# Kernel optimization log

Hardware: AMD Instinct MI355X
Metric: run time of the kernel (lower is better)

Reference implementation:

```python
import jax, jax.numpy as jnp
import numpy as np

B, N, D_IN, D_OUT = 2, 2048, 2048, 2048
H, G = 16, 4            # num_heads, n_kv_groups
HD = D_OUT // H         # head_dim = 128
REP = H // G            # query heads per kv head = 4


def setup_inputs() -> dict:
    key = jax.random.key(0)
    ks = jax.random.split(key, 6)
    s = lambda fan_in: 1.0 / np.sqrt(fan_in)
    return {
        "x": jax.random.normal(ks[0], (B, N, D_IN), jnp.float32),
        "Wq": jax.random.normal(ks[1], (D_IN, D_OUT), jnp.float32) * s(D_IN),
        "Wk": jax.random.normal(ks[2], (D_IN, G * HD), jnp.float32) * s(D_IN),
        "Wv": jax.random.normal(ks[3], (D_IN, G * HD), jnp.float32) * s(D_IN),
        "Wo": jax.random.normal(ks[4], (D_OUT, D_OUT), jnp.float32) * s(D_OUT),
        "bo": jnp.zeros((D_OUT,), jnp.float32),
    }


def reference(x, Wq, Wk, Wv, Wo, bo):
    b, n, _ = x.shape
    # projections
    q = (x @ Wq).reshape(b, n, G, REP, HD)   # query heads grouped: h = g*REP + r
    k = (x @ Wk).reshape(b, n, G, HD)
    v = (x @ Wv).reshape(b, n, G, HD)
    # grouped attention scores; KV broadcast over REP instead of repeat_kv
    scores = jnp.einsum('bqgrd,bkgd->bgrqk', q, k)  # [b,G,REP,N,N]
    causal = jnp.tril(jnp.ones((n, n), bool))       # allowed positions
    scores = jnp.where(causal, scores, -jnp.inf)
    w = jax.nn.softmax(scores / np.float32(np.sqrt(HD)), axis=-1)
    ctx = jnp.einsum('bgrqk,bkgd->bqgrd', w, v).reshape(b, n, D_OUT)
    return ctx @ Wo + bo
```

## Files before the change

kernel.cpp:

```cpp
#include <hip/hip_runtime.h>
#include <stdint.h>

typedef __attribute__((ext_vector_type(8))) __bf16 bf16x8;
typedef __attribute__((ext_vector_type(4))) float f32x4;
typedef __attribute__((ext_vector_type(4))) short short4v;

static constexpr int SEQ  = 2048;
static constexpr int DQKV = 3072;
static constexpr int HD   = 128;

__device__ __forceinline__ short f2bf(float f) {
  unsigned u = __builtin_bit_cast(unsigned, f);
  u += 0x7fffu + ((u >> 16) & 1u);
  return (short)(u >> 16);
}

__device__ __forceinline__ unsigned pack2(float a, float b) {
  return (unsigned)(unsigned short)f2bf(a) | ((unsigned)(unsigned short)f2bf(b) << 16);
}

__device__ __forceinline__ void gl_lds16(const void* g, void* l) {
  __builtin_amdgcn_global_load_lds(
      (const __attribute__((address_space(1))) void*)g,
      (__attribute__((address_space(3))) void*)l, 16, 0, 0);
}

__global__ __launch_bounds__(256)
void prep_kernel(const float* __restrict__ x, const float* __restrict__ Wq,
                 const float* __restrict__ Wk, const float* __restrict__ Wv,
                 const float* __restrict__ Wo,
                 short* __restrict__ xb, short* __restrict__ WqkvT,
                 short* __restrict__ WoT) {
  int blk = blockIdx.x, tid = threadIdx.x;
  if (blk < 8192) {
    int i = blk * 256 + tid;
    float4 v = reinterpret_cast<const float4*>(x)[i];
    short4v o;
    o[0] = f2bf(v.x); o[1] = f2bf(v.y); o[2] = f2bf(v.z); o[3] = f2bf(v.w);
    *reinterpret_cast<short4v*>(xb + (size_t)i * 4) = o;
    return;
  }
  blk -= 8192;
  __shared__ float tile[32][33];
  const float* in; short* out; int C, bx, by;
  if (blk < 4096)      { in = Wq; out = WqkvT;                     C = 2048; bx = blk & 63; by = blk >> 6; }
  else if (blk < 5120) { int t = blk - 4096; in = Wk; out = WqkvT + (size_t)2048 * 2048; C = 512; bx = t & 15; by = t >> 4; }
  else if (blk < 6144) { int t = blk - 5120; in = Wv; out = WqkvT + (size_t)2560 * 2048; C = 512; bx = t & 15; by = t >> 4; }
  else                 { int t = blk - 6144; in = Wo; out = WoT;   C = 2048; bx = t & 63; by = t >> 6; }
  const int R = 2048;
  int c0 = bx * 32, r0 = by * 32, tx = tid & 31, ty = tid >> 5;
  for (int i = 0; i < 4; i++)
    tile[ty + i * 8][tx] = in[(size_t)(r0 + ty + i * 8) * C + c0 + tx];
  __syncthreads();
  for (int i = 0; i < 4; i++)
    out[(size_t)(c0 + ty + i * 8) * R + r0 + tx] = f2bf(tile[tx][ty + i * 8]);
}

__global__ __launch_bounds__(256) void transpose_v_kernel(const short* __restrict__ qkv,
                                                          short* __restrict__ vT) {
  __shared__ short tile[32][33];
  int n0 = blockIdx.x * 32, c0 = blockIdx.y * 32, b = blockIdx.z;
  int tx = threadIdx.x & 31, ty = threadIdx.x >> 5;
  for (int i = 0; i < 4; i++)
    tile[ty + i * 8][tx] = qkv[(size_t)(b * SEQ + n0 + ty + i * 8) * DQKV + 2560 + c0 + tx];
  __syncthreads();
  for (int i = 0; i < 4; i++)
    vT[(size_t)(b * 512 + c0 + ty + i * 8) * SEQ + n0 + tx] = tile[tx][ty + i * 8];
}

template <int F32OUT>
__global__ __launch_bounds__(256)
void gemm_bt_kernel(const short* __restrict__ A, const short* __restrict__ BT,
                    void* __restrict__ Cout, const float* __restrict__ bias,
                    int M, int N, int K, int qcols, float qscale) {
  __shared__ __align__(16) short As[8192];
  __shared__ __align__(16) short Bs[8192];
  const int tid = threadIdx.x, lane = tid & 63, w = tid >> 6;
  const int l15 = lane & 15, quad = lane >> 4, q8 = quad * 8;
  const int row0 = blockIdx.y * 128, col0 = blockIdx.x * 128;
  const int wm = (w >> 1) * 64, wn = (w & 1) * 64;
  f32x4 acc[4][4] = {};
  const short* ga0 = A  + (size_t)(row0 + w * 16 + (lane >> 2)) * K + (lane & 3) * 8;
  const short* gb0 = BT + (size_t)(col0 + w * 16 + (lane >> 2)) * K + (lane & 3) * 8;
  for (int kt = 0; kt < K; kt += 64) {
    for (int s = 0; s < 2; s++) {
      gl_lds16(ga0 + kt + s * 32,                  As + s * 4096 + w * 512);
      gl_lds16(ga0 + (size_t)64 * K + kt + s * 32, As + s * 4096 + 2048 + w * 512);
      gl_lds16(gb0 + kt + s * 32,                  Bs + s * 4096 + w * 512);
      gl_lds16(gb0 + (size_t)64 * K + kt + s * 32, Bs + s * 4096 + 2048 + w * 512);
    }
    __syncthreads();
    for (int s = 0; s < 2; s++) {
      bf16x8 af[4], bfr[4];
      for (int i = 0; i < 4; i++)
        af[i] = *reinterpret_cast<const bf16x8*>(As + s * 4096 + (wm + i * 16 + l15) * 32 + q8);
      for (int j = 0; j < 4; j++)
        bfr[j] = *reinterpret_cast<const bf16x8*>(Bs + s * 4096 + (wn + j * 16 + l15) * 32 + q8);
      for (int i = 0; i < 4; i++)
        for (int j = 0; j < 4; j++)
          acc[i][j] = __builtin_amdgcn_mfma_f32_16x16x32_bf16(af[i], bfr[j], acc[i][j], 0, 0, 0);
    }
    __syncthreads();
  }
  if (F32OUT) {
    float* C = (float*)Cout;
    for (int j = 0; j < 4; j++) {
      int col = col0 + wn + j * 16 + l15;
      float bv = bias[col];
      for (int i = 0; i < 4; i++)
        for (int r = 0; r < 4; r++)
          C[(size_t)(row0 + wm + i * 16 + quad * 4 + r) * N + col] = acc[i][j][r] + bv;
    }
  } else {
    short* C = (short*)Cout;
    for (int j = 0; j < 4; j++) {
      int col = col0 + wn + j * 16 + l15;
      float sc = (col < qcols) ? qscale : 1.0f;
      for (int i = 0; i < 4; i++)
        for (int r = 0; r < 4; r++)
          C[(size_t)(row0 + wm + i * 16 + quad * 4 + r) * N + col] = f2bf(acc[i][j][r] * sc);
    }
  }
}

__global__ __launch_bounds__(512, 4)
void attn_kernel(const short* __restrict__ qkv, const short* __restrict__ vT,
                 short* __restrict__ ctx) {
  __shared__ __align__(16) short Ks[16384];
  __shared__ __align__(16) short Vs[16384];
  __shared__ __align__(16) short Ps[8192];
  const int tid = threadIdx.x, lane = tid & 63, w = tid >> 6;
  const int l15 = lane & 15, quad = lane >> 4, q8 = quad * 8;
  const int idx = blockIdx.x;
  const int qt = 15 - (idx >> 5);
  const int h = (idx >> 1) & 15, b = idx & 1, g = h >> 2;

  bf16x8 qf[4];
  {
    const short* gq = qkv + (size_t)(b * SEQ + qt * 128 + w * 16 + l15) * DQKV + h * HD + q8;
    for (int ds = 0; ds < 4; ds++)
      qf[ds] = *reinterpret_cast<const bf16x8*>(gq + ds * 32);
  }
  bf16x8 ones;
  for (int i = 0; i < 8; i++) ones[i] = __builtin_bit_cast(__bf16, (short)0x3F80);

  f32x4 acco[8] = {};
  f32x4 accl = {};

  auto stage = [&](int buf, int kt) {
    if (w < 4) {
      const short* gk = qkv + (size_t)(b * SEQ + kt * 64 + w * 16 + (lane >> 2)) * DQKV +
                        2048 + g * HD + (lane & 3) * 8;
      for (int ks = 0; ks < 4; ks++)
        gl_lds16(gk + ks * 32, Ks + buf * 8192 + ks * 2048 + w * 512);
    } else {
      const int w4 = w - 4;
      for (int c = 0; c < 2; c++)
        for (int ih = 0; ih < 2; ih++)
          gl_lds16(vT + (size_t)(b * 512 + g * HD + ih * 64 + w4 * 16 + (lane >> 2)) * SEQ +
                       kt * 64 + c * 32 + (lane & 3) * 8,
                   Vs + buf * 8192 + c * 4096 + ih * 2048 + w4 * 512);
    }
  };

  const int kmax = 2 * qt + 1;
  stage(0, 0);
  for (int kt = 0; kt <= kmax; kt++) {
    const int cur = kt & 1;
    __syncthreads();
    if (kt < kmax) stage(cur ^ 1, kt + 1);

    const short* Kb = Ks + cur * 8192;
    const short* Vb = Vs + cur * 8192;

    f32x4 accs[4] = {};
    for (int ds = 0; ds < 4; ds++)
      for (int j = 0; j < 4; j++) {
        bf16x8 kf = *reinterpret_cast<const bf16x8*>(Kb + ds * 2048 + (j * 16 + l15) * 32 + q8);
        accs[j] = __builtin_amdgcn_mfma_f32_16x16x32_bf16(kf, qf[ds], accs[j], 0, 0, 0);
      }

    if (kt >= 2 * qt) {
      const int qm = qt * 128 + w * 16 + l15 - kt * 64;
      for (int j = 0; j < 4; j++)
        for (int r = 0; r < 4; r++)
          if (j * 16 + quad * 4 + r > qm) accs[j][r] = -1e38f;
    }

    for (int j = 0; j < 4; j++) {
      float p0 = exp2f(accs[j][0]), p1 = exp2f(accs[j][1]);
      float p2 = exp2f(accs[j][2]), p3 = exp2f(accs[j][3]);
      unsigned u0 = __builtin_bit_cast(unsigned, p0), u1 = __builtin_bit_cast(unsigned, p1);
      unsigned u2 = __builtin_bit_cast(unsigned, p2), u3 = __builtin_bit_cast(unsigned, p3);
      uint2 dd = make_uint2((u0 >> 16) | (u1 & 0xffff0000u),
                            (u2 >> 16) | (u3 & 0xffff0000u));
      const int chw = (2 * j + (quad >> 1)) ^ (l15 & 7);
      *reinterpret_cast<uint2*>(Ps + w * 1024 + l15 * 64 + chw * 8 + (quad & 1) * 4) = dd;
    }
    asm volatile("s_waitcnt lgkmcnt(0)" ::: "memory");

    for (int c = 0; c < 2; c++) {
      const int chr = (4 * c + quad) ^ (l15 & 7);
      bf16x8 pf = *reinterpret_cast<const bf16x8*>(Ps + w * 1024 + l15 * 64 + chr * 8);
      accl = __builtin_amdgcn_mfma_f32_16x16x32_bf16(ones, pf, accl, 0, 0, 0);
      for (int nt = 0; nt < 8; nt++) {
        bf16x8 vf = *reinterpret_cast<const bf16x8*>(Vb + c * 4096 + (nt * 16 + l15) * 32 + q8);
        acco[nt] = __builtin_amdgcn_mfma_f32_16x16x32_bf16(vf, pf, acco[nt], 0, 0, 0);
      }
    }
  }

  const float invl = 1.f / accl[0];
  const size_t row = (size_t)(b * SEQ + qt * 128 + w * 16 + l15);
  for (int nt = 0; nt < 8; nt++) {
    uint2 dd = make_uint2(pack2(acco[nt][0] * invl, acco[nt][1] * invl),
                          pack2(acco[nt][2] * invl, acco[nt][3] * invl));
    *reinterpret_cast<uint2*>(ctx + row * 2048 + h * HD + nt * 16 + quad * 4) = dd;
  }
}

extern "C" void kernel_launch(void* const* d_in, const int* in_sizes, int n_in,
                              void* d_out, int out_size, void* d_ws, size_t ws_size,
                              hipStream_t stream) {
  const float* x  = (const float*)d_in[0];
  const float* Wq = (const float*)d_in[1];
  const float* Wk = (const float*)d_in[2];
  const float* Wv = (const float*)d_in[3];
  const float* Wo = (const float*)d_in[4];
  const float* bo = (const float*)d_in[5];
  float* out = (float*)d_out;

  const float sc2 = 0.08838834764831845f * 1.4426950408889634f;

  short* xb    = (short*)d_ws;
  short* WqkvT = xb    + (size_t)4096 * 2048;
  short* WoT   = WqkvT + (size_t)3072 * 2048;
  short* qkv   = WoT   + (size_t)2048 * 2048;
  short* vT    = qkv   + (size_t)4096 * 3072;
  short* ctx   = vT    + (size_t)1024 * 2048;

  prep_kernel<<<dim3(18432), dim3(256), 0, stream>>>(x, Wq, Wk, Wv, Wo, xb, WqkvT, WoT);
  gemm_bt_kernel<0><<<dim3(24, 32), dim3(256), 0, stream>>>(xb, WqkvT, qkv, nullptr,
                                                            4096, 3072, 2048, 2048, sc2);
  transpose_v_kernel<<<dim3(64, 16, 2), dim3(256), 0, stream>>>(qkv, vT);
  attn_kernel<<<dim3(512), dim3(512), 0, stream>>>(qkv, vT, ctx);
  gemm_bt_kernel<1><<<dim3(16, 32), dim3(256), 0, stream>>>(ctx, WoT, out, bo,
                                                            4096, 2048, 2048, 0, 1.0f);
}
```

Measured before the change: 306.1 us.

## Pair complementary 64-row query tiles per attention block for causal load balance

The attention kernel now uses 256-thread blocks, each handling two 64-row query tiles (p and 31-p) processed back to back. Every block therefore walks the same number of K/V tiles, which evens out the causal triangle workload across blocks. Previously each block had a single 128-row tile with work varying by tile. In exchange, each block keeps fewer waves, and K/V tiles are staged once per 64 query rows instead of per 128 rows, which raises memory traffic per unit of compute.

```diff
diff --git a/kernel.cpp b/kernel.cpp
--- a/kernel.cpp
+++ b/kernel.cpp
@@ -123,23 +123,24 @@
   }
 }
 
-__global__ __launch_bounds__(512, 4)
+__global__ __launch_bounds__(256, 2)
 void attn_kernel(const short* __restrict__ qkv, const short* __restrict__ vT,
                  short* __restrict__ ctx) {
   __shared__ __align__(16) short Ks[16384];
   __shared__ __align__(16) short Vs[16384];
-  __shared__ __align__(16) short Ps[8192];
+  __shared__ __align__(16) short Ps[4096];
   const int tid = threadIdx.x, lane = tid & 63, w = tid >> 6;
   const int l15 = lane & 15, quad = lane >> 4, q8 = quad * 8;
   const int idx = blockIdx.x;
-  const int qt = 15 - (idx >> 5);
-  const int h = (idx >> 1) & 15, b = idx & 1, g = h >> 2;
-
-  bf16x8 qf[4];
-  {
-    const short* gq = qkv + (size_t)(b * SEQ + qt * 128 + w * 16 + l15) * DQKV + h * HD + q8;
+  const int p = idx >> 5, h = (idx >> 1) & 15, b = idx & 1, g = h >> 2;
+  const int qtA = 31 - p, qtB = p;
+
+  bf16x8 qf[2][4];
+  for (int seg = 0; seg < 2; seg++) {
+    const int qt = seg ? qtB : qtA;
+    const short* gq = qkv + (size_t)(b * SEQ + qt * 64 + w * 16 + l15) * DQKV + h * HD + q8;
     for (int ds = 0; ds < 4; ds++)
-      qf[ds] = *reinterpret_cast<const bf16x8*>(gq + ds * 32);
+      qf[seg][ds] = *reinterpret_cast<const bf16x8*>(gq + ds * 32);
   }
   bf16x8 ones;
   for (int i = 0; i < 8; i++) ones[i] = __builtin_bit_cast(__bf16, (short)0x3F80);
@@ -148,27 +149,30 @@
   f32x4 accl = {};
 
   auto stage = [&](int buf, int kt) {
-    if (w < 4) {
-      const short* gk = qkv + (size_t)(b * SEQ + kt * 64 + w * 16 + (lane >> 2)) * DQKV +
-                        2048 + g * HD + (lane & 3) * 8;
-      for (int ks = 0; ks < 4; ks++)
-        gl_lds16(gk + ks * 32, Ks + buf * 8192 + ks * 2048 + w * 512);
-    } else {
-      const int w4 = w - 4;
-      for (int c = 0; c < 2; c++)
-        for (int ih = 0; ih < 2; ih++)
-          gl_lds16(vT + (size_t)(b * 512 + g * HD + ih * 64 + w4 * 16 + (lane >> 2)) * SEQ +
-                       kt * 64 + c * 32 + (lane & 3) * 8,
-                   Vs + buf * 8192 + c * 4096 + ih * 2048 + w4 * 512);
-    }
+    const short* gk = qkv + (size_t)(b * SEQ + kt * 64 + w * 16 + (lane >> 2)) * DQKV +
+                      2048 + g * HD + (lane & 3) * 8;
+    for (int ks = 0; ks < 4; ks++)
+      gl_lds16(gk + ks * 32, Ks + buf * 8192 + ks * 2048 + w * 512);
+    for (int c = 0; c < 2; c++)
+      for (int ih = 0; ih < 2; ih++)
+        gl_lds16(vT + (size_t)(b * 512 + g * HD + ih * 64 + w * 16 + (lane >> 2)) * SEQ +
+                     kt * 64 + c * 32 + (lane & 3) * 8,
+                 Vs + buf * 8192 + c * 4096 + ih * 2048 + w * 512);
   };
 
-  const int kmax = 2 * qt + 1;
+  const int lenA = qtA + 1;
+  const int total = lenA + qtB + 1;
   stage(0, 0);
-  for (int kt = 0; kt <= kmax; kt++) {
-    const int cur = kt & 1;
+  for (int t = 0; t < total; t++) {
+    const int seg = (t >= lenA);
+    const int kt = seg ? (t - lenA) : t;
+    const int qt = seg ? qtB : qtA;
+    const int cur = t & 1;
     __syncthreads();
-    if (kt < kmax) stage(cur ^ 1, kt + 1);
+    if (t + 1 < total) {
+      const int nkt = (t + 1 >= lenA) ? (t + 1 - lenA) : (t + 1);
+      stage(cur ^ 1, nkt);
+    }
 
     const short* Kb = Ks + cur * 8192;
     const short* Vb = Vs + cur * 8192;
@@ -177,14 +181,14 @@
     for (int ds = 0; ds < 4; ds++)
       for (int j = 0; j < 4; j++) {
         bf16x8 kf = *reinterpret_cast<const bf16x8*>(Kb + ds * 2048 + (j * 16 + l15) * 32 + q8);
-        accs[j] = __builtin_amdgcn_mfma_f32_16x16x32_bf16(kf, qf[ds], accs[j], 0, 0, 0);
+        accs[j] = __builtin_amdgcn_mfma_f32_16x16x32_bf16(kf, qf[seg][ds], accs[j], 0, 0, 0);
       }
 
-    if (kt >= 2 * qt) {
-      const int qm = qt * 128 + w * 16 + l15 - kt * 64;
+    if (kt == qt) {
+      const int q = w * 16 + l15;
       for (int j = 0; j < 4; j++)
         for (int r = 0; r < 4; r++)
-          if (j * 16 + quad * 4 + r > qm) accs[j][r] = -1e38f;
+          if (j * 16 + quad * 4 + r > q) accs[j][r] = -1e38f;
     }
 
     for (int j = 0; j < 4; j++) {
@@ -208,14 +212,18 @@
         acco[nt] = __builtin_amdgcn_mfma_f32_16x16x32_bf16(vf, pf, acco[nt], 0, 0, 0);
       }
     }
-  }
-
-  const float invl = 1.f / accl[0];
-  const size_t row = (size_t)(b * SEQ + qt * 128 + w * 16 + l15);
-  for (int nt = 0; nt < 8; nt++) {
-    uint2 dd = make_uint2(pack2(acco[nt][0] * invl, acco[nt][1] * invl),
-                          pack2(acco[nt][2] * invl, acco[nt][3] * invl));
-    *reinterpret_cast<uint2*>(ctx + row * 2048 + h * HD + nt * 16 + quad * 4) = dd;
+
+    if (kt == qt) {
+      const float invl = 1.f / accl[0];
+      const size_t row = (size_t)(b * SEQ + qt * 64 + w * 16 + l15);
+      for (int nt = 0; nt < 8; nt++) {
+        uint2 dd = make_uint2(pack2(acco[nt][0] * invl, acco[nt][1] * invl),
+                              pack2(acco[nt][2] * invl, acco[nt][3] * invl));
+        *reinterpret_cast<uint2*>(ctx + row * 2048 + h * HD + nt * 16 + quad * 4) = dd;
+      }
+      for (int nt = 0; nt < 8; nt++) acco[nt] = f32x4{0.f, 0.f, 0.f, 0.f};
+      accl = f32x4{0.f, 0.f, 0.f, 0.f};
+    }
   }
 }
 
@@ -243,7 +251,7 @@
   gemm_bt_kernel<0><<<dim3(24, 32), dim3(256), 0, stream>>>(xb, WqkvT, qkv, nullptr,
                                                             4096, 3072, 2048, 2048, sc2);
   transpose_v_kernel<<<dim3(64, 16, 2), dim3(256), 0, stream>>>(qkv, vT);
-  attn_kernel<<<dim3(512), dim3(512), 0, stream>>>(qkv, vT, ctx);
+  attn_kernel<<<dim3(512), dim3(256), 0, stream>>>(qkv, vT, ctx);
   gemm_bt_kernel<1><<<dim3(16, 32), dim3(256), 0, stream>>>(ctx, WoT, out, bo,
                                                             4096, 2048, 2048, 0, 1.0f);
 }
```

Measured after the change: 287.6 us. 1.06x faster.
